# Kernel tuning notes

Measured on AMD Instinct MI355X. Metric: run time of the kernel, lower is better.

## Reference

```python
import jax, jax.numpy as jnp
import numpy as np

B, T, VOCAB, EMBED, HID, TAGS = 64, 512, 30000, 512, 1024, 48
H1, H2 = HID // 2, HID // 4  # per-direction hidden sizes of lstm_1 / lstm_2


def setup_inputs() -> dict:
    key = jax.random.key(0)
    ks = iter(jax.random.split(key, 40))
    def rn(shape, s=0.05):
        return jax.random.normal(next(ks), shape, dtype=jnp.float32) * s
    inp = {
        "sequences": jax.random.randint(next(ks), (B, T), 0, VOCAB),
        "tags": jax.random.randint(next(ks), (B, T), 0, TAGS),
        "mask": jnp.ones((B, T), dtype=bool),
        "h0": rn((2, B, H1), 1.0), "c0": rn((2, B, H1), 1.0),
        "h1": rn((2, B, H2), 1.0), "c1": rn((2, B, H2), 1.0),
        "embed_table": rn((VOCAB, EMBED), 1.0),
        "lin_w": rn((TAGS, 2 * H2)), "lin_b": rn((TAGS,)),
        "transitions": rn((TAGS, TAGS)),
        "start_trans": rn((TAGS,)), "end_trans": rn((TAGS,)),
    }
    for name, (i_dim, h_dim) in {"1f": (EMBED, H1), "1b": (EMBED, H1),
                                 "2f": (2 * H1, H2), "2b": (2 * H1, H2)}.items():
        inp["w_ih" + name] = rn((4 * h_dim, i_dim))
        inp["w_hh" + name] = rn((4 * h_dim, h_dim))
        inp["b_ih" + name] = rn((4 * h_dim,))
        inp["b_hh" + name] = rn((4 * h_dim,))
    return inp


def _lstm_scan(x, h0, c0, w_ih, w_hh, b):
    # x: [T,B,I] time-major; PyTorch gate order i,f,g,o
    def step(carry, x_t):
        h, c = carry
        g = x_t @ w_ih.T + h @ w_hh.T + b  # [B,4H]
        i, f, gg, o = jnp.split(g, 4, axis=-1)
        c = jax.nn.sigmoid(f) * c + jax.nn.sigmoid(i) * jnp.tanh(gg)
        h = jax.nn.sigmoid(o) * jnp.tanh(c)
        return (h, c), h
    _, hs = jax.lax.scan(step, (h0, c0), x)
    return hs  # [T,B,H]


def _bilstm(x, h0, c0, pf, pb):
    hf = _lstm_scan(x, h0[0], c0[0], *pf)
    hb = _lstm_scan(x[::-1], h0[1], c0[1], *pb)[::-1]
    return jnp.concatenate([hf, hb], axis=-1)


def _crf_partition(logits, mask, trans, start, end):
    # logits: [T,B,K], mask: [T,B] bool -> log Z per example [B]
    alpha0 = start[None, :] + logits[0]
    def step(alpha, inp):
        emit, m = inp
        inner = alpha[:, :, None] + trans[None, :, :] + emit[:, None, :]
        new = jax.nn.logsumexp(inner, axis=1)
        return jnp.where(m[:, None], new, alpha), None
    alpha, _ = jax.lax.scan(step, alpha0, (logits[1:], mask[1:]))
    return jax.nn.logsumexp(alpha + end[None, :], axis=-1)


def _crf_joint(logits, tags, mask, trans, start, end):
    # logits: [T,B,K], tags/mask: [T,B] -> gold path score [B]
    mf = mask.astype(logits.dtype)
    bidx = jnp.arange(tags.shape[1])
    emit = jnp.take_along_axis(logits, tags[..., None], axis=-1)[..., 0]  # [T,B]
    score = start[tags[0]]
    score = score + jnp.sum(trans[tags[:-1], tags[1:]] * mf[1:], axis=0)
    score = score + jnp.sum(emit[:-1] * mf[:-1], axis=0)
    last_idx = jnp.sum(mask.astype(jnp.int32), axis=0) - 1
    last_tags = tags[last_idx, bidx]
    score = score + end[last_tags] + logits[-1, bidx, last_tags] * mf[-1]
    return score


def reference(sequences, tags, mask, h0, c0, h1, c1, embed_table, lin_w, lin_b,
              transitions, start_trans, end_trans,
              w_ih1f, w_hh1f, b_ih1f, b_hh1f, w_ih1b, w_hh1b, b_ih1b, b_hh1b,
              w_ih2f, w_hh2f, b_ih2f, b_hh2f, w_ih2b, w_hh2b, b_ih2b, b_hh2b):
    x = embed_table[sequences.T]  # [T,B,E] (time-major, as in get_logits)
    out1 = _bilstm(x, h0, c0,
                   (w_ih1f, w_hh1f, b_ih1f + b_hh1f),
                   (w_ih1b, w_hh1b, b_ih1b + b_hh1b))  # [T,B,HID]
    out2 = _bilstm(out1, h1, c1,
                   (w_ih2f, w_hh2f, b_ih2f + b_hh2f),
                   (w_ih2b, w_hh2b, b_ih2b + b_hh2b))  # [T,B,HID//2]
    logits = out2 @ lin_w.T + lin_b  # [T,B,TAGS]; dropout is identity in eval
    mt, tt = mask.T, tags.T  # [T,B]
    log_z = _crf_partition(logits, mt, transitions, start_trans, end_trans)
    joint = _crf_joint(logits, tt, mt, transitions, start_trans, end_trans)
    return -jnp.sum(joint - log_z)
```

## Files before the change

### kernel.cpp

```cpp
#include <hip/hip_runtime.h>
#include <stdint.h>

#define TT 512
#define BB 64
#define NTAGS 48
#define CH 64

typedef __attribute__((ext_vector_type(8))) short bf16x8;
typedef __attribute__((ext_vector_type(4))) float f32x4;
typedef __attribute__((ext_vector_type(4))) unsigned short u16x4;

__device__ inline unsigned short f2bf(float f) {
  union { float f; unsigned u; } v; v.f = f;
  unsigned r = v.u + 0x7fffu + ((v.u >> 16) & 1u);
  return (unsigned short)(r >> 16);
}
__device__ inline float bf2f(unsigned short u) {
  union { unsigned u; float f; } v; v.u = ((unsigned)u) << 16; return v.f;
}
__device__ inline float sigf(float x) { return 1.0f / (1.0f + __expf(-x)); }
__device__ inline float tanhfast(float x) { return 1.0f - 2.0f / (__expf(2.0f * x) + 1.0f); }

__global__ void k_gather_x(const float* __restrict__ emb, const int* __restrict__ seq,
                           unsigned short* __restrict__ x) {
  size_t i4 = ((size_t)blockIdx.x * 256 + threadIdx.x) * 4;
  int r = (int)(i4 >> 9);
  int k = (int)(i4 & 511);
  int t = r >> 6, b = r & 63;
  int tok = seq[b * TT + t];
  float4 v = *(const float4*)(emb + (size_t)tok * 512 + k);
  unsigned short* dst = x + i4;
  dst[0] = f2bf(v.x); dst[1] = f2bf(v.y); dst[2] = f2bf(v.z); dst[3] = f2bf(v.w);
}

__global__ void k_conv(const float* __restrict__ s, unsigned short* __restrict__ d, int n4) {
  int i = blockIdx.x * 256 + threadIdx.x;
  if (i >= n4) return;
  float4 v = *(const float4*)(s + (size_t)i * 4);
  unsigned short* dst = d + (size_t)i * 4;
  dst[0] = f2bf(v.x); dst[1] = f2bf(v.y); dst[2] = f2bf(v.z); dst[3] = f2bf(v.w);
}

__global__ void k_misc2(const float* __restrict__ h0, const float* __restrict__ h1,
                        const float* __restrict__ c0, const float* __restrict__ c1,
                        const float* __restrict__ bi1f, const float* __restrict__ bh1f,
                        const float* __restrict__ bi1b, const float* __restrict__ bh1b,
                        const float* __restrict__ bi2f, const float* __restrict__ bh2f,
                        const float* __restrict__ bi2b, const float* __restrict__ bh2b,
                        float* __restrict__ bs1, float* __restrict__ bs2,
                        unsigned short* __restrict__ hb1, unsigned short* __restrict__ hb2,
                        float* __restrict__ cb1, float* __restrict__ cb2) {
  int i = blockIdx.x * 256 + threadIdx.x;
  if (i < 4096) { int dd = i >> 11, n = i & 2047; bs1[i] = dd ? (bi1b[n] + bh1b[n]) : (bi1f[n] + bh1f[n]); return; }
  i -= 4096;
  if (i < 2048) { int dd = i >> 10, n = i & 1023; bs2[i] = dd ? (bi2b[n] + bh2b[n]) : (bi2f[n] + bh2f[n]); return; }
  i -= 2048;
  if (i < 65536) { hb1[i] = f2bf(h0[i]); return; }
  i -= 65536;
  if (i < 32768) { hb2[i] = f2bf(h1[i]); return; }
  i -= 32768;
  if (i < 65536) { cb1[i] = c0[i]; return; }
  i -= 65536;
  if (i < 32768) { cb2[i] = c1[i]; return; }
}

template<int KX, int H>
__global__ __launch_bounds__(512) void k_xproj_c(
    const unsigned short* __restrict__ xin,
    const unsigned short* __restrict__ Wih,
    const float* __restrict__ bsum,
    unsigned short* __restrict__ xp, int s0) {
  const int UG = H / 16;
  int wid = blockIdx.x * 8 + (threadIdx.x >> 6);
  const int lane = threadIdx.x & 63;
  const int ug = wid % UG; wid /= UG;
  const int g = wid & 3; wid >>= 2;
  const int dir = wid & 1; wid >>= 1;
  const int sc = wid;
  const int s = s0 + sc;
  const int t = dir ? (TT - 1 - s) : s;
  const int r16 = lane & 15, kg = lane >> 4;
  const int rowg = dir * 4 * H + g * H + ug * 16 + r16;
  const unsigned short* wrow = Wih + (size_t)rowg * KX + kg * 8;
  const float bias = bsum[rowg];
  const unsigned short* xa = xin + (size_t)t * 64 * KX + kg * 8;
  f32x4 A0 = {bias, bias, bias, bias}, A1 = A0, A2 = A0, A3 = A0;
  #pragma unroll
  for (int kc = 0; kc < KX / 128; ++kc) {
    bf16x8 wv_[4], av_[4][4];
    #pragma unroll
    for (int u = 0; u < 4; ++u) {
      const int kk = kc * 4 + u;
      wv_[u] = *(const bf16x8*)(wrow + kk * 32);
      av_[u][0] = *(const bf16x8*)(xa + (size_t)(0 * 16 + r16) * KX + kk * 32);
      av_[u][1] = *(const bf16x8*)(xa + (size_t)(1 * 16 + r16) * KX + kk * 32);
      av_[u][2] = *(const bf16x8*)(xa + (size_t)(2 * 16 + r16) * KX + kk * 32);
      av_[u][3] = *(const bf16x8*)(xa + (size_t)(3 * 16 + r16) * KX + kk * 32);
    }
    #pragma unroll
    for (int u = 0; u < 4; ++u) {
      A0 = __builtin_amdgcn_mfma_f32_16x16x32_bf16(av_[u][0], wv_[u], A0, 0, 0, 0);
      A1 = __builtin_amdgcn_mfma_f32_16x16x32_bf16(av_[u][1], wv_[u], A1, 0, 0, 0);
      A2 = __builtin_amdgcn_mfma_f32_16x16x32_bf16(av_[u][2], wv_[u], A2, 0, 0, 0);
      A3 = __builtin_amdgcn_mfma_f32_16x16x32_bf16(av_[u][3], wv_[u], A3, 0, 0, 0);
    }
  }
  unsigned short* dst = xp + ((((size_t)sc * 2 + dir) * UG + ug) * 4 + g) * 1024 + lane * 4;
  u16x4 s0v = {f2bf(A0[0]), f2bf(A0[1]), f2bf(A0[2]), f2bf(A0[3])};
  u16x4 s1v = {f2bf(A1[0]), f2bf(A1[1]), f2bf(A1[2]), f2bf(A1[3])};
  u16x4 s2v = {f2bf(A2[0]), f2bf(A2[1]), f2bf(A2[2]), f2bf(A2[3])};
  u16x4 s3v = {f2bf(A3[0]), f2bf(A3[1]), f2bf(A3[2]), f2bf(A3[3])};
  *(u16x4*)(dst + 0)   = s0v;
  *(u16x4*)(dst + 256) = s1v;
  *(u16x4*)(dst + 512) = s2v;
  *(u16x4*)(dst + 768) = s3v;
}

template<int H, int NBLKD>
__global__ __launch_bounds__(256, 1) void k_lstm_c(
    const unsigned short* __restrict__ xp,
    const unsigned short* __restrict__ Whh,
    float* __restrict__ cbuf,
    unsigned short* __restrict__ hbuf,
    unsigned short* __restrict__ outp,
    unsigned* __restrict__ arr, int s0) {
  const int UG = H / 16;
  const int dir = blockIdx.x / NBLKD;
  const int ug  = blockIdx.x % NBLKD;
  const int bt = threadIdx.x >> 6, lane = threadIdx.x & 63;
  const int r16 = lane & 15, kg = lane >> 4;

  __shared__ unsigned short Wl[64 * H];
  for (int c = threadIdx.x; c < 64 * (H / 8); c += 256) {
    const int lrow = c / (H / 8), k8 = c % (H / 8);
    bf16x8 v = *(const bf16x8*)(Whh + ((size_t)(dir * 4 * H + (lrow >> 4) * H + ug * 16 + (lrow & 15))) * H + k8 * 8);
    const int addr = ((lrow * H + k8 * 8) * 2) ^ ((lrow & 7) << 4);
    *(bf16x8*)((char*)Wl + addr) = v;
  }

  const int batch0 = bt * 16 + kg * 4;
  float creg[4];
  #pragma unroll
  for (int rr = 0; rr < 4; ++rr)
    creg[rr] = cbuf[((size_t)dir * 64 + batch0 + rr) * H + ug * 16 + r16];

  __syncthreads();

  unsigned* const grp    = arr + (size_t)(dir * 4 + bt) * NBLKD * 4;
  unsigned* const myflag = grp + (size_t)ug * 4;

  auto xpb = [&](int sc) -> const unsigned short* {
    return xp + (((size_t)sc * 2 + dir) * UG + ug) * 4096 + bt * 256 + lane * 4;
  };
  const unsigned short* pb = xpb(0);
  u16x4 px0 = *(const u16x4*)(pb + 0);
  u16x4 px1 = *(const u16x4*)(pb + 1024);
  u16x4 px2 = *(const u16x4*)(pb + 2048);
  u16x4 px3 = *(const u16x4*)(pb + 3072);

  for (int sc = 0; sc < CH; ++sc) {
    const int s = s0 + sc;
    const int p = s & 1;
    f32x4 A0, A1, A2, A3;
    #pragma unroll
    for (int rr = 0; rr < 4; ++rr) {
      A0[rr] = bf2f(px0[rr]);
      A1[rr] = bf2f(px1[rr]);
      A2[rr] = bf2f(px2[rr]);
      A3[rr] = bf2f(px3[rr]);
    }
    if (sc + 1 < CH) {
      pb = xpb(sc + 1);
      px0 = *(const u16x4*)(pb + 0);
      px1 = *(const u16x4*)(pb + 1024);
      px2 = *(const u16x4*)(pb + 2048);
      px3 = *(const u16x4*)(pb + 3072);
    }
    if (s > 0) {
      const unsigned* ap = grp + (size_t)lane * 4;
      const bool act = lane < NBLKD;
      for (;;) {
        unsigned vv = act ? __hip_atomic_load(ap, __ATOMIC_RELAXED, __HIP_MEMORY_SCOPE_AGENT)
                          : 0xffffffffu;
        if (__all(vv >= (unsigned)s)) break;
        __builtin_amdgcn_s_sleep(1);
      }
      asm volatile("" ::: "memory");
    }
    const unsigned short* hrow = hbuf + (((size_t)p * 2 + dir) * 64 + bt * 16 + r16) * H + kg * 8;
    bf16x8 hreg[H / 32];
    #pragma unroll
    for (int kk = 0; kk < H / 32; ++kk) {
      union { bf16x8 v; unsigned long long q[2]; } hu;
      hu.q[0] = __hip_atomic_load((const unsigned long long*)(hrow + kk * 32), __ATOMIC_RELAXED, __HIP_MEMORY_SCOPE_AGENT);
      hu.q[1] = __hip_atomic_load((const unsigned long long*)(hrow + kk * 32 + 4), __ATOMIC_RELAXED, __HIP_MEMORY_SCOPE_AGENT);
      hreg[kk] = hu.v;
    }
    const int sw = (r16 & 7) << 4;
    #pragma unroll
    for (int kk = 0; kk < H / 32; ++kk) {
      bf16x8 w0 = *(const bf16x8*)((const char*)Wl + ((((0 * 16 + r16) * H + kk * 32 + kg * 8) * 2) ^ sw));
      bf16x8 w1 = *(const bf16x8*)((const char*)Wl + ((((1 * 16 + r16) * H + kk * 32 + kg * 8) * 2) ^ sw));
      bf16x8 w2 = *(const bf16x8*)((const char*)Wl + ((((2 * 16 + r16) * H + kk * 32 + kg * 8) * 2) ^ sw));
      bf16x8 w3 = *(const bf16x8*)((const char*)Wl + ((((3 * 16 + r16) * H + kk * 32 + kg * 8) * 2) ^ sw));
      A0 = __builtin_amdgcn_mfma_f32_16x16x32_bf16(hreg[kk], w0, A0, 0, 0, 0);
      A1 = __builtin_amdgcn_mfma_f32_16x16x32_bf16(hreg[kk], w1, A1, 0, 0, 0);
      A2 = __builtin_amdgcn_mfma_f32_16x16x32_bf16(hreg[kk], w2, A2, 0, 0, 0);
      A3 = __builtin_amdgcn_mfma_f32_16x16x32_bf16(hreg[kk], w3, A3, 0, 0, 0);
    }
    const int t = dir ? (TT - 1 - s) : s;
    unsigned short* hw = hbuf + ((size_t)(p ^ 1) * 2 + dir) * 64 * H;
    unsigned short hbv[4];
    #pragma unroll
    for (int rr = 0; rr < 4; ++rr) {
      float cn = sigf(A1[rr]) * creg[rr] + sigf(A0[rr]) * tanhfast(A2[rr]);
      float hn = sigf(A3[rr]) * tanhfast(cn);
      creg[rr] = cn;
      hbv[rr] = f2bf(hn);
      __hip_atomic_store(hw + (size_t)(batch0 + rr) * H + ug * 16 + r16, hbv[rr],
                         __ATOMIC_RELAXED, __HIP_MEMORY_SCOPE_AGENT);
    }
    asm volatile("s_waitcnt vmcnt(0)" ::: "memory");
    if (lane == 0)
      __hip_atomic_store(myflag, (unsigned)(s + 1), __ATOMIC_RELAXED, __HIP_MEMORY_SCOPE_AGENT);
    #pragma unroll
    for (int rr = 0; rr < 4; ++rr)
      outp[((size_t)t * 64 + batch0 + rr) * (2 * H) + dir * H + ug * 16 + r16] = hbv[rr];
  }
  #pragma unroll
  for (int rr = 0; rr < 4; ++rr)
    cbuf[((size_t)dir * 64 + batch0 + rr) * H + ug * 16 + r16] = creg[rr];
}

template<int KX, int H, int NBLKD>
__global__ __launch_bounds__(512, 2) void k_lstm(
    const unsigned short* __restrict__ xin, const unsigned short* __restrict__ Wih,
    const unsigned short* __restrict__ Whh, const float* __restrict__ bsum,
    const float* __restrict__ cinit, unsigned short* __restrict__ hbuf,
    unsigned short* __restrict__ outp, unsigned* __restrict__ arr) {
  const int dir = blockIdx.x / NBLKD;
  const int ug  = blockIdx.x % NBLKD;
  const int wv = threadIdx.x >> 6, lane = threadIdx.x & 63;
  const int r16 = lane & 15, kg = lane >> 4;
  __shared__ unsigned short Wl[64 * H];
  __shared__ float xacc[2][4][4][256];
  __shared__ unsigned done[2];
  __shared__ int ready;
  if (threadIdx.x == 0) { done[0] = 0u; done[1] = 0u; ready = -1; }
  for (int c = threadIdx.x; c < 64 * (H / 8); c += 512) {
    const int lrow = c / (H / 8), k8 = c % (H / 8);
    bf16x8 v = *(const bf16x8*)(Whh + ((size_t)(dir * 4 * H + (lrow >> 4) * H + ug * 16 + (lrow & 15))) * H + k8 * 8);
    const int addr = ((lrow * H + k8 * 8) * 2) ^ ((lrow & 7) << 4);
    *(bf16x8*)((char*)Wl + addr) = v;
  }
  float creg[4];
  auto xgemm = [&](int sn) {
    const int gg = wv - 4;
    const int rowg = dir * 4 * H + gg * H + ug * 16 + r16;
    const unsigned short* wrow = Wih + (size_t)rowg * KX + kg * 8;
    const float bias = bsum[rowg];
    const int t = dir ? (TT - 1 - sn) : sn;
    const unsigned short* xa = xin + (size_t)t * 64 * KX + kg * 8;
    f32x4 A0 = {bias, bias, bias, bias}, A1 = A0, A2 = A0, A3 = A0;
    #pragma unroll
    for (int kc = 0; kc < KX / 128; ++kc) {
      bf16x8 wv_[4], av_[4][4];
      #pragma unroll
      for (int u = 0; u < 4; ++u) {
        const int kk = kc * 4 + u;
        wv_[u] = *(const bf16x8*)(wrow + kk * 32);
        av_[u][0] = *(const bf16x8*)(xa + (size_t)(0 * 16 + r16) * KX + kk * 32);
        av_[u][1] = *(const bf16x8*)(xa + (size_t)(1 * 16 + r16) * KX + kk * 32);
        av_[u][2] = *(const bf16x8*)(xa + (size_t)(2 * 16 + r16) * KX + kk * 32);
        av_[u][3] = *(const bf16x8*)(xa + (size_t)(3 * 16 + r16) * KX + kk * 32);
      }
      #pragma unroll
      for (int u = 0; u < 4; ++u) {
        A0 = __builtin_amdgcn_mfma_f32_16x16x32_bf16(av_[u][0], wv_[u], A0, 0, 0, 0);
        A1 = __builtin_amdgcn_mfma_f32_16x16x32_bf16(av_[u][1], wv_[u], A1, 0, 0, 0);
        A2 = __builtin_amdgcn_mfma_f32_16x16x32_bf16(av_[u][2], wv_[u], A2, 0, 0, 0);
        A3 = __builtin_amdgcn_mfma_f32_16x16x32_bf16(av_[u][3], wv_[u], A3, 0, 0, 0);
      }
    }
    const int p = sn & 1;
    *(f32x4*)&xacc[p][gg][0][lane * 4] = A0;
    *(f32x4*)&xacc[p][gg][1][lane * 4] = A1;
    *(f32x4*)&xacc[p][gg][2][lane * 4] = A2;
    *(f32x4*)&xacc[p][gg][3][lane * 4] = A3;
  };
  if (wv < 4) {
    const int batch0 = wv * 16 + kg * 4;
    #pragma unroll
    for (int rr = 0; rr < 4; ++rr)
      creg[rr] = cinit[((size_t)dir * 64 + batch0 + rr) * H + ug * 16 + r16];
  } else {
    xgemm(0);
  }
  for (int s = 0; s < TT; ++s) {
    __syncthreads();
    if (wv >= 4) {
      if (s + 1 < TT) xgemm(s + 1);
    } else {
      const int p = s & 1;
      const int bt = wv;
      f32x4 A0 = *(const f32x4*)&xacc[p][0][bt][lane * 4];
      f32x4 A1 = *(const f32x4*)&xacc[p][1][bt][lane * 4];
      f32x4 A2 = *(const f32x4*)&xacc[p][2][bt][lane * 4];
      f32x4 A3 = *(const f32x4*)&xacc[p][3][bt][lane * 4];
      const unsigned short* hrow = hbuf + (((size_t)p * 2 + dir) * 64 + bt * 16 + r16) * H + kg * 8;
      if (s > 0) {
        if (wv == 0) {
          const unsigned* ap = arr + ((size_t)dir * NBLKD + lane) * 4;
          const bool act = lane < NBLKD;
          for (;;) {
            unsigned vv = act ? __hip_atomic_load(ap, __ATOMIC_RELAXED, __HIP_MEMORY_SCOPE_AGENT)
                              : 0xffffffffu;
            if (__all(vv >= (unsigned)s)) break;
            __builtin_amdgcn_s_sleep(4);
          }
          if (lane == 0) __hip_atomic_store(&ready, s, __ATOMIC_RELAXED, __HIP_MEMORY_SCOPE_WORKGROUP);
        } else {
          while (__hip_atomic_load(&ready, __ATOMIC_RELAXED, __HIP_MEMORY_SCOPE_WORKGROUP) < s)
            __builtin_amdgcn_s_sleep(1);
        }
        asm volatile("" ::: "memory");
      }
      bf16x8 hreg[H / 32];
      #pragma unroll
      for (int kk = 0; kk < H / 32; ++kk) {
        union { bf16x8 v; unsigned long long q[2]; } hu;
        hu.q[0] = __hip_atomic_load((const unsigned long long*)(hrow + kk * 32), __ATOMIC_RELAXED, __HIP_MEMORY_SCOPE_AGENT);
        hu.q[1] = __hip_atomic_load((const unsigned long long*)(hrow + kk * 32 + 4), __ATOMIC_RELAXED, __HIP_MEMORY_SCOPE_AGENT);
        hreg[kk] = hu.v;
      }
      const int sw = (r16 & 7) << 4;
      #pragma unroll
      for (int kk = 0; kk < H / 32; ++kk) {
        bf16x8 w0 = *(const bf16x8*)((const char*)Wl + ((((0 * 16 + r16) * H + kk * 32 + kg * 8) * 2) ^ sw));
        bf16x8 w1 = *(const bf16x8*)((const char*)Wl + ((((1 * 16 + r16) * H + kk * 32 + kg * 8) * 2) ^ sw));
        bf16x8 w2 = *(const bf16x8*)((const char*)Wl + ((((2 * 16 + r16) * H + kk * 32 + kg * 8) * 2) ^ sw));
        bf16x8 w3 = *(const bf16x8*)((const char*)Wl + ((((3 * 16 + r16) * H + kk * 32 + kg * 8) * 2) ^ sw));
        A0 = __builtin_amdgcn_mfma_f32_16x16x32_bf16(hreg[kk], w0, A0, 0, 0, 0);
        A1 = __builtin_amdgcn_mfma_f32_16x16x32_bf16(hreg[kk], w1, A1, 0, 0, 0);
        A2 = __builtin_amdgcn_mfma_f32_16x16x32_bf16(hreg[kk], w2, A2, 0, 0, 0);
        A3 = __builtin_amdgcn_mfma_f32_16x16x32_bf16(hreg[kk], w3, A3, 0, 0, 0);
      }
      const int t = dir ? (TT - 1 - s) : s;
      const int batch0 = bt * 16 + kg * 4;
      unsigned short* hw = hbuf + ((size_t)(p ^ 1) * 2 + dir) * 64 * H;
      unsigned short hbv[4];
      #pragma unroll
      for (int rr = 0; rr < 4; ++rr) {
        float cn = sigf(A1[rr]) * creg[rr] + sigf(A0[rr]) * tanhfast(A2[rr]);
        float hn = sigf(A3[rr]) * tanhfast(cn);
        creg[rr] = cn;
        hbv[rr] = f2bf(hn);
        __hip_atomic_store(hw + (size_t)(batch0 + rr) * H + ug * 16 + r16, hbv[rr],
                           __ATOMIC_RELAXED, __HIP_MEMORY_SCOPE_AGENT);
      }
      asm volatile("s_waitcnt vmcnt(0)" ::: "memory");
      if (lane == 0) {
        unsigned old = __hip_atomic_fetch_add(&done[p], 1u, __ATOMIC_ACQ_REL, __HIP_MEMORY_SCOPE_WORKGROUP);
        if (old == 3u) {
          done[p] = 0u;
          __hip_atomic_store(arr + ((size_t)dir * NBLKD + ug) * 4, (unsigned)(s + 1),
                             __ATOMIC_RELAXED, __HIP_MEMORY_SCOPE_AGENT);
        }
      }
      #pragma unroll
      for (int rr = 0; rr < 4; ++rr)
        outp[((size_t)t * 64 + batch0 + rr) * (2 * H) + dir * H + ug * 16 + r16] = hbv[rr];
    }
  }
}

__global__ __launch_bounds__(256) void k_linear(const unsigned short* __restrict__ out2,
                                                const unsigned short* __restrict__ wl,
                                                const float* __restrict__ lb,
                                                float* __restrict__ logits) {
  const int wid = blockIdx.x * 4 + (threadIdx.x >> 6);
  const int lane = threadIdx.x & 63;
  const int mt = wid / 3, nt = wid % 3;
  const int r16 = lane & 15, kg = lane >> 4;
  const unsigned short* ar = out2 + ((size_t)mt * 16 + r16) * 512 + kg * 8;
  const unsigned short* br = wl + ((size_t)(nt * 16 + r16)) * 512 + kg * 8;
  f32x4 acc = {0.f, 0.f, 0.f, 0.f};
  #pragma unroll
  for (int kk = 0; kk < 16; ++kk) {
    bf16x8 av = *(const bf16x8*)(ar + kk * 32);
    bf16x8 bv = *(const bf16x8*)(br + kk * 32);
    acc = __builtin_amdgcn_mfma_f32_16x16x32_bf16(av, bv, acc, 0, 0, 0);
  }
  const int col = nt * 16 + r16;
  const float bias = lb[col];
  #pragma unroll
  for (int rr = 0; rr < 4; ++rr) {
    const int m = mt * 16 + kg * 4 + rr;
    logits[(size_t)m * 48 + col] = acc[rr] + bias;
  }
}

__global__ void k_crf_part(const float* __restrict__ logits, const float* __restrict__ trans,
                           const float* __restrict__ start, const float* __restrict__ endt,
                           float* __restrict__ logz) {
  const int b = blockIdx.x;
  const int j = threadIdx.x;
  __shared__ __align__(16) float alpha[2][NTAGS];
  float trj[NTAGS];
  if (j < NTAGS) {
    #pragma unroll
    for (int i = 0; i < NTAGS; ++i) trj[i] = trans[i * NTAGS + j];
    alpha[0][j] = start[j] + logits[(size_t)b * NTAGS + j];
  }
  float cur = (j < NTAGS) ? logits[((size_t)1 * BB + b) * NTAGS + j] : 0.f;
  __syncthreads();
  for (int t = 1; t < TT; ++t) {
    float nxt = (j < NTAGS && t + 1 < TT) ? logits[((size_t)(t + 1) * BB + b) * NTAGS + j] : 0.f;
    const int p = (t - 1) & 1;
    float newv = 0.f;
    if (j < NTAGS) {
      float v[NTAGS];
      const float4* ap = (const float4*)&alpha[p][0];
      #pragma unroll
      for (int q = 0; q < NTAGS / 4; ++q) {
        float4 v4 = ap[q];
        v[4 * q + 0] = v4.x + trj[4 * q + 0];
        v[4 * q + 1] = v4.y + trj[4 * q + 1];
        v[4 * q + 2] = v4.z + trj[4 * q + 2];
        v[4 * q + 3] = v4.w + trj[4 * q + 3];
      }
      float m0[24], m1[12], m2[6], m3[3];
      #pragma unroll
      for (int i = 0; i < 24; ++i) m0[i] = fmaxf(v[2 * i], v[2 * i + 1]);
      #pragma unroll
      for (int i = 0; i < 12; ++i) m1[i] = fmaxf(m0[2 * i], m0[2 * i + 1]);
      #pragma unroll
      for (int i = 0; i < 6; ++i) m2[i] = fmaxf(m1[2 * i], m1[2 * i + 1]);
      #pragma unroll
      for (int i = 0; i < 3; ++i) m3[i] = fmaxf(m2[2 * i], m2[2 * i + 1]);
      const float m = fmaxf(fmaxf(m3[0], m3[1]), m3[2]);
      float e[NTAGS];
      #pragma unroll
      for (int i = 0; i < NTAGS; ++i) e[i] = __expf(v[i] - m);
      float s0[24], s1[12], s2[6], s3[3];
      #pragma unroll
      for (int i = 0; i < 24; ++i) s0[i] = e[2 * i] + e[2 * i + 1];
      #pragma unroll
      for (int i = 0; i < 12; ++i) s1[i] = s0[2 * i] + s0[2 * i + 1];
      #pragma unroll
      for (int i = 0; i < 6; ++i) s2[i] = s1[2 * i] + s1[2 * i + 1];
      #pragma unroll
      for (int i = 0; i < 3; ++i) s3[i] = s2[2 * i] + s2[2 * i + 1];
      const float ssum = s3[0] + s3[1] + s3[2];
      newv = m + __logf(ssum) + cur;
    }
    if (j < NTAGS) alpha[p ^ 1][j] = newv;
    __syncthreads();
    cur = nxt;
  }
  float vfin = (j < NTAGS) ? alpha[(TT - 1) & 1][j] + endt[j] : -1e30f;
  float m = vfin;
  for (int o = 32; o; o >>= 1) m = fmaxf(m, __shfl_xor(m, o));
  float e = (j < NTAGS) ? __expf(vfin - m) : 0.f;
  for (int o = 32; o; o >>= 1) e += __shfl_xor(e, o);
  if (j == 0) logz[b] = m + __logf(e);
}

__global__ void k_crf_joint(const float* __restrict__ logits, const int* __restrict__ tags,
                            const float* __restrict__ trans, const float* __restrict__ start,
                            const float* __restrict__ endt, float* __restrict__ joint) {
  const int b = blockIdx.x;
  const int tid = threadIdx.x;
  float p = 0.f;
  for (int t = tid; t < TT - 1; t += 64) {
    const int tt = tags[b * TT + t], tn = tags[b * TT + t + 1];
    p += trans[tt * NTAGS + tn] + logits[((size_t)t * BB + b) * 48 + tt];
  }
  for (int o = 32; o; o >>= 1) p += __shfl_xor(p, o);
  if (tid == 0) {
    const int t0 = tags[b * TT];
    const int tl = tags[b * TT + TT - 1];
    p += start[t0] + endt[tl] + logits[((size_t)(TT - 1) * BB + b) * 48 + tl];
    joint[b] = p;
  }
}

__global__ void k_final(const float* __restrict__ joint, const float* __restrict__ logz,
                        float* __restrict__ out) {
  const int tid = threadIdx.x;
  float v = joint[tid] - logz[tid];
  for (int o = 32; o; o >>= 1) v += __shfl_xor(v, o);
  if (tid == 0) out[0] = -v;
}

#define X_OFF    ((size_t)0)
#define WIH1_OFF ((size_t)33554432)
#define WHH1_OFF ((size_t)37748736)
#define WIH2_OFF ((size_t)41943040)
#define WHH2_OFF ((size_t)46137344)
#define WL_OFF   ((size_t)47185920)
#define BS1_OFF  ((size_t)47235072)
#define BS2_OFF  ((size_t)47251456)
#define OUT1_OFF ((size_t)47259648)
#define OUT2_OFF ((size_t)114368512)
#define LG_OFF   ((size_t)147922944)
#define HB1_OFF  ((size_t)154214400)
#define HB2_OFF  ((size_t)154476544)
#define LZ_OFF   ((size_t)154607616)
#define JT_OFF   ((size_t)154607872)
#define BAR_OFF  ((size_t)154608128)
#define WS_NEED  ((size_t)154624512)
#define CB1_OFF  ((size_t)154624512)
#define CB2_OFF  ((size_t)154886656)
#define XP_OFF   ((size_t)155017728)
#define WS_XP    ((size_t)171794944)

extern "C" void kernel_launch(void* const* d_in, const int* in_sizes, int n_in,
                              void* d_out, int out_size, void* d_ws, size_t ws_size,
                              hipStream_t stream) {
  if (ws_size < WS_NEED) return;
  const int*   seq    = (const int*)d_in[0];
  const int*   tags   = (const int*)d_in[1];
  const float* h0     = (const float*)d_in[3];
  const float* c0     = (const float*)d_in[4];
  const float* h1     = (const float*)d_in[5];
  const float* c1     = (const float*)d_in[6];
  const float* emb    = (const float*)d_in[7];
  const float* lin_w  = (const float*)d_in[8];
  const float* lin_b  = (const float*)d_in[9];
  const float* trans  = (const float*)d_in[10];
  const float* start_t= (const float*)d_in[11];
  const float* end_t  = (const float*)d_in[12];
  const float* wih1f  = (const float*)d_in[13];
  const float* whh1f  = (const float*)d_in[14];
  const float* bih1f  = (const float*)d_in[15];
  const float* bhh1f  = (const float*)d_in[16];
  const float* wih1b  = (const float*)d_in[17];
  const float* whh1b  = (const float*)d_in[18];
  const float* bih1b  = (const float*)d_in[19];
  const float* bhh1b  = (const float*)d_in[20];
  const float* wih2f  = (const float*)d_in[21];
  const float* whh2f  = (const float*)d_in[22];
  const float* bih2f  = (const float*)d_in[23];
  const float* bhh2f  = (const float*)d_in[24];
  const float* wih2b  = (const float*)d_in[25];
  const float* whh2b  = (const float*)d_in[26];
  const float* bih2b  = (const float*)d_in[27];
  const float* bhh2b  = (const float*)d_in[28];

  char* ws = (char*)d_ws;
  unsigned short* x    = (unsigned short*)(ws + X_OFF);
  unsigned short* Wih1 = (unsigned short*)(ws + WIH1_OFF);
  unsigned short* Whh1 = (unsigned short*)(ws + WHH1_OFF);
  unsigned short* Wih2 = (unsigned short*)(ws + WIH2_OFF);
  unsigned short* Whh2 = (unsigned short*)(ws + WHH2_OFF);
  unsigned short* WL   = (unsigned short*)(ws + WL_OFF);
  float*          bs1  = (float*)(ws + BS1_OFF);
  float*          bs2  = (float*)(ws + BS2_OFF);
  unsigned short* out1 = (unsigned short*)(ws + OUT1_OFF);
  unsigned short* out2 = (unsigned short*)(ws + OUT2_OFF);
  float*          lg   = (float*)(ws + LG_OFF);
  unsigned short* hb1  = (unsigned short*)(ws + HB1_OFF);
  unsigned short* hb2  = (unsigned short*)(ws + HB2_OFF);
  float*          lz   = (float*)(ws + LZ_OFF);
  float*          jt   = (float*)(ws + JT_OFF);
  unsigned*       bars = (unsigned*)(ws + BAR_OFF);
  const bool big = ws_size >= WS_XP;
  float*          cb1  = big ? (float*)(ws + CB1_OFF) : nullptr;
  float*          cb2  = big ? (float*)(ws + CB2_OFF) : nullptr;
  unsigned short* xp   = big ? (unsigned short*)(ws + XP_OFF) : nullptr;

  hipMemsetAsync(bars, 0, 16384, stream);

  k_gather_x<<<16384, 256, 0, stream>>>(emb, seq, x);
  k_conv<<<1024, 256, 0, stream>>>(wih1f, Wih1,                 262144);
  k_conv<<<1024, 256, 0, stream>>>(wih1b, Wih1 + 2048 * 512,    262144);
  k_conv<<<1024, 256, 0, stream>>>(whh1f, Whh1,                 262144);
  k_conv<<<1024, 256, 0, stream>>>(whh1b, Whh1 + 2048 * 512,    262144);
  k_conv<<<1024, 256, 0, stream>>>(wih2f, Wih2,                 262144);
  k_conv<<<1024, 256, 0, stream>>>(wih2b, Wih2 + 1024 * 1024,   262144);
  k_conv<<<256, 256, 0, stream>>>(whh2f, Whh2,                  65536);
  k_conv<<<256, 256, 0, stream>>>(whh2b, Whh2 + 1024 * 256,     65536);
  k_conv<<<24, 256, 0, stream>>>(lin_w, WL,                     6144);

  if (big) {
    k_misc2<<<792, 256, 0, stream>>>(h0, h1, c0, c1, bih1f, bhh1f, bih1b, bhh1b,
                                     bih2f, bhh2f, bih2b, bhh2b, bs1, bs2, hb1, hb2, cb1, cb2);
    for (int c = 0; c < TT / CH; ++c) {
      k_xproj_c<512, 512><<<2048, 512, 0, stream>>>(x, Wih1, bs1, xp, c * CH);
      k_lstm_c<512, 32><<<64, 256, 0, stream>>>(xp, Whh1, cb1, hb1, out1, bars, c * CH);
    }
    for (int c = 0; c < TT / CH; ++c) {
      k_xproj_c<1024, 256><<<1024, 512, 0, stream>>>(out1, Wih2, bs2, xp, c * CH);
      k_lstm_c<256, 16><<<32, 256, 0, stream>>>(xp, Whh2, cb2, hb2, out2, bars + 2048, c * CH);
    }
  } else {
    k_misc2<<<792, 256, 0, stream>>>(h0, h1, c0, c1, bih1f, bhh1f, bih1b, bhh1b,
                                     bih2f, bhh2f, bih2b, bhh2b, bs1, bs2, hb1, hb2,
                                     (float*)(ws + LG_OFF), (float*)(ws + LG_OFF + 262144));
    k_lstm<512, 512, 32><<<64, 512, 0, stream>>>(x, Wih1, Whh1, bs1, c0, hb1, out1, bars);
    k_lstm<1024, 256, 16><<<32, 512, 0, stream>>>(out1, Wih2, Whh2, bs2, c1, hb2, out2, bars + 1024);
  }

  k_linear<<<1536, 256, 0, stream>>>(out2, WL, lin_b, lg);
  k_crf_part<<<64, 64, 0, stream>>>(lg, trans, start_t, end_t, lz);
  k_crf_joint<<<64, 64, 0, stream>>>(lg, tags, trans, start_t, end_t, jt);
  k_final<<<1, 64, 0, stream>>>(jt, lz, (float*)d_out);
}
```

Measured before the change: 7.704 ms.

## Fuse next-chunk input projection into LSTM recurrence kernel and tag hidden state with step

The recurrence kernel and the input projection for the next time chunk now share one launch. Extra blocks beyond the recurrent ones compute the next chunk's projections into a double-buffered area while the persistent blocks run the sequential steps at raised priority. The per-block flag barrier is replaced by hidden-state words that carry the step index in their upper 16 bits, so consumers spin directly on the data. This removes the separate flag store, the waitcnt and the flag polling, at the cost of doubling hidden-state storage and needing more workspace. The projection blocks also compete with the latency-critical recurrent blocks for memory bandwidth.

```diff
diff --git a/kernel.cpp b/kernel.cpp
--- a/kernel.cpp
+++ b/kernel.cpp
@@ -49,7 +49,8 @@
                         const float* __restrict__ bi2b, const float* __restrict__ bh2b,
                         float* __restrict__ bs1, float* __restrict__ bs2,
                         unsigned short* __restrict__ hb1, unsigned short* __restrict__ hb2,
-                        float* __restrict__ cb1, float* __restrict__ cb2) {
+                        float* __restrict__ cb1, float* __restrict__ cb2,
+                        unsigned* __restrict__ hb1u, unsigned* __restrict__ hb2u) {
   int i = blockIdx.x * 256 + threadIdx.x;
   if (i < 4096) { int dd = i >> 11, n = i & 2047; bs1[i] = dd ? (bi1b[n] + bh1b[n]) : (bi1f[n] + bh1f[n]); return; }
   i -= 4096;
@@ -62,14 +63,16 @@
   if (i < 65536) { cb1[i] = c0[i]; return; }
   i -= 65536;
   if (i < 32768) { cb2[i] = c1[i]; return; }
+  i -= 32768;
+  if (i < 65536) { if (hb1u) hb1u[i] = (unsigned)f2bf(h0[i]); return; }
+  i -= 65536;
+  if (i < 32768) { if (hb2u) hb2u[i] = (unsigned)f2bf(h1[i]); return; }
 }
 
 template<int KX, int H>
 __global__ __launch_bounds__(512) void k_xproj_c(
-    const unsigned short* __restrict__ xin,
-    const unsigned short* __restrict__ Wih,
-    const float* __restrict__ bsum,
-    unsigned short* __restrict__ xp, int s0) {
+    const unsigned short* __restrict__ xin, const unsigned short* __restrict__ Wih,
+    const float* __restrict__ bsum, unsigned short* __restrict__ xp, int s0) {
   const int UG = H / 16;
   int wid = blockIdx.x * 8 + (threadIdx.x >> 6);
   const int lane = threadIdx.x & 63;
@@ -116,15 +119,70 @@
   *(u16x4*)(dst + 768) = s3v;
 }
 
-template<int H, int NBLKD>
-__global__ __launch_bounds__(256, 1) void k_lstm_c(
-    const unsigned short* __restrict__ xp,
+template<int KX, int H, int NBLKD>
+__global__ __launch_bounds__(256, 1) void k_fused(
+    const unsigned short* __restrict__ xin,
+    const unsigned short* __restrict__ Wih,
+    const float* __restrict__ bsum,
+    unsigned short* __restrict__ xpw,
+    const unsigned short* __restrict__ xpr,
     const unsigned short* __restrict__ Whh,
     float* __restrict__ cbuf,
-    unsigned short* __restrict__ hbuf,
+    unsigned* __restrict__ hbu,
     unsigned short* __restrict__ outp,
-    unsigned* __restrict__ arr, int s0) {
+    int s0, int xs0) {
   const int UG = H / 16;
+  const int NL = 2 * NBLKD;
+
+  if ((int)blockIdx.x >= NL) {
+    if (!xpw) return;
+    const int wv = threadIdx.x >> 6, lane = threadIdx.x & 63;
+    int wid = ((int)blockIdx.x - NL) * 4 + wv;
+    const int ug = wid % UG; wid /= UG;
+    const int g = wid & 3; wid >>= 2;
+    const int dir = wid & 1; wid >>= 1;
+    const int sc = wid;
+    const int s = xs0 + sc;
+    const int t = dir ? (TT - 1 - s) : s;
+    const int r16 = lane & 15, kg = lane >> 4;
+    const int rowg = dir * 4 * H + g * H + ug * 16 + r16;
+    const unsigned short* wrow = Wih + (size_t)rowg * KX + kg * 8;
+    const float bias = bsum[rowg];
+    const unsigned short* xa = xin + (size_t)t * 64 * KX + kg * 8;
+    f32x4 A0 = {bias, bias, bias, bias}, A1 = A0, A2 = A0, A3 = A0;
+    #pragma unroll
+    for (int kc = 0; kc < KX / 128; ++kc) {
+      bf16x8 wv_[4], av_[4][4];
+      #pragma unroll
+      for (int u = 0; u < 4; ++u) {
+        const int kk = kc * 4 + u;
+        wv_[u] = *(const bf16x8*)(wrow + kk * 32);
+        av_[u][0] = *(const bf16x8*)(xa + (size_t)(0 * 16 + r16) * KX + kk * 32);
+        av_[u][1] = *(const bf16x8*)(xa + (size_t)(1 * 16 + r16) * KX + kk * 32);
+        av_[u][2] = *(const bf16x8*)(xa + (size_t)(2 * 16 + r16) * KX + kk * 32);
+        av_[u][3] = *(const bf16x8*)(xa + (size_t)(3 * 16 + r16) * KX + kk * 32);
+      }
+      #pragma unroll
+      for (int u = 0; u < 4; ++u) {
+        A0 = __builtin_amdgcn_mfma_f32_16x16x32_bf16(av_[u][0], wv_[u], A0, 0, 0, 0);
+        A1 = __builtin_amdgcn_mfma_f32_16x16x32_bf16(av_[u][1], wv_[u], A1, 0, 0, 0);
+        A2 = __builtin_amdgcn_mfma_f32_16x16x32_bf16(av_[u][2], wv_[u], A2, 0, 0, 0);
+        A3 = __builtin_amdgcn_mfma_f32_16x16x32_bf16(av_[u][3], wv_[u], A3, 0, 0, 0);
+      }
+    }
+    unsigned short* dst = xpw + ((((size_t)sc * 2 + dir) * UG + ug) * 4 + g) * 1024 + lane * 4;
+    u16x4 s0v = {f2bf(A0[0]), f2bf(A0[1]), f2bf(A0[2]), f2bf(A0[3])};
+    u16x4 s1v = {f2bf(A1[0]), f2bf(A1[1]), f2bf(A1[2]), f2bf(A1[3])};
+    u16x4 s2v = {f2bf(A2[0]), f2bf(A2[1]), f2bf(A2[2]), f2bf(A2[3])};
+    u16x4 s3v = {f2bf(A3[0]), f2bf(A3[1]), f2bf(A3[2]), f2bf(A3[3])};
+    *(u16x4*)(dst + 0)   = s0v;
+    *(u16x4*)(dst + 256) = s1v;
+    *(u16x4*)(dst + 512) = s2v;
+    *(u16x4*)(dst + 768) = s3v;
+    return;
+  }
+
+  __builtin_amdgcn_s_setprio(1);
   const int dir = blockIdx.x / NBLKD;
   const int ug  = blockIdx.x % NBLKD;
   const int bt = threadIdx.x >> 6, lane = threadIdx.x & 63;
@@ -146,11 +204,8 @@
 
   __syncthreads();
 
-  unsigned* const grp    = arr + (size_t)(dir * 4 + bt) * NBLKD * 4;
-  unsigned* const myflag = grp + (size_t)ug * 4;
-
   auto xpb = [&](int sc) -> const unsigned short* {
-    return xp + (((size_t)sc * 2 + dir) * UG + ug) * 4096 + bt * 256 + lane * 4;
+    return xpr + (((size_t)sc * 2 + dir) * UG + ug) * 4096 + bt * 256 + lane * 4;
   };
   const unsigned short* pb = xpb(0);
   u16x4 px0 = *(const u16x4*)(pb + 0);
@@ -176,40 +231,49 @@
       px2 = *(const u16x4*)(pb + 2048);
       px3 = *(const u16x4*)(pb + 3072);
     }
-    if (s > 0) {
-      const unsigned* ap = grp + (size_t)lane * 4;
-      const bool act = lane < NBLKD;
-      for (;;) {
-        unsigned vv = act ? __hip_atomic_load(ap, __ATOMIC_RELAXED, __HIP_MEMORY_SCOPE_AGENT)
-                          : 0xffffffffu;
-        if (__all(vv >= (unsigned)s)) break;
-        __builtin_amdgcn_s_sleep(1);
-      }
-      asm volatile("" ::: "memory");
-    }
-    const unsigned short* hrow = hbuf + (((size_t)p * 2 + dir) * 64 + bt * 16 + r16) * H + kg * 8;
-    bf16x8 hreg[H / 32];
+    const unsigned* hrowu = hbu + (((size_t)p * 2 + dir) * 64 + bt * 16 + r16) * H + kg * 8;
+    unsigned hr[H / 32][4];
+    const unsigned exp_hi = (unsigned)s << 16;
+    for (;;) {
+      unsigned bad = 0u;
+      #pragma unroll
+      for (int kk = 0; kk < H / 32; ++kk) {
+        unsigned long long q0 = __hip_atomic_load((const unsigned long long*)(hrowu + kk * 32 + 0), __ATOMIC_RELAXED, __HIP_MEMORY_SCOPE_AGENT);
+        unsigned long long q1 = __hip_atomic_load((const unsigned long long*)(hrowu + kk * 32 + 2), __ATOMIC_RELAXED, __HIP_MEMORY_SCOPE_AGENT);
+        unsigned long long q2 = __hip_atomic_load((const unsigned long long*)(hrowu + kk * 32 + 4), __ATOMIC_RELAXED, __HIP_MEMORY_SCOPE_AGENT);
+        unsigned long long q3 = __hip_atomic_load((const unsigned long long*)(hrowu + kk * 32 + 6), __ATOMIC_RELAXED, __HIP_MEMORY_SCOPE_AGENT);
+        unsigned w0 = (unsigned)q0, w1 = (unsigned)(q0 >> 32);
+        unsigned w2 = (unsigned)q1, w3 = (unsigned)(q1 >> 32);
+        unsigned w4 = (unsigned)q2, w5 = (unsigned)(q2 >> 32);
+        unsigned w6 = (unsigned)q3, w7 = (unsigned)(q3 >> 32);
+        bad |= (w0 ^ exp_hi) | (w1 ^ exp_hi) | (w2 ^ exp_hi) | (w3 ^ exp_hi)
+             | (w4 ^ exp_hi) | (w5 ^ exp_hi) | (w6 ^ exp_hi) | (w7 ^ exp_hi);
+        hr[kk][0] = (w0 & 0xFFFFu) | (w1 << 16);
+        hr[kk][1] = (w2 & 0xFFFFu) | (w3 << 16);
+        hr[kk][2] = (w4 & 0xFFFFu) | (w5 << 16);
+        hr[kk][3] = (w6 & 0xFFFFu) | (w7 << 16);
+      }
+      if (__all((bad & 0xFFFF0000u) == 0u)) break;
+      __builtin_amdgcn_s_sleep(1);
+    }
+    const int sw = (r16 & 7) << 4;
     #pragma unroll
     for (int kk = 0; kk < H / 32; ++kk) {
-      union { bf16x8 v; unsigned long long q[2]; } hu;
-      hu.q[0] = __hip_atomic_load((const unsigned long long*)(hrow + kk * 32), __ATOMIC_RELAXED, __HIP_MEMORY_SCOPE_AGENT);
-      hu.q[1] = __hip_atomic_load((const unsigned long long*)(hrow + kk * 32 + 4), __ATOMIC_RELAXED, __HIP_MEMORY_SCOPE_AGENT);
-      hreg[kk] = hu.v;
-    }
-    const int sw = (r16 & 7) << 4;
-    #pragma unroll
-    for (int kk = 0; kk < H / 32; ++kk) {
+      union { unsigned u[4]; bf16x8 v; } hu;
+      hu.u[0] = hr[kk][0]; hu.u[1] = hr[kk][1]; hu.u[2] = hr[kk][2]; hu.u[3] = hr[kk][3];
+      bf16x8 av = hu.v;
       bf16x8 w0 = *(const bf16x8*)((const char*)Wl + ((((0 * 16 + r16) * H + kk * 32 + kg * 8) * 2) ^ sw));
       bf16x8 w1 = *(const bf16x8*)((const char*)Wl + ((((1 * 16 + r16) * H + kk * 32 + kg * 8) * 2) ^ sw));
       bf16x8 w2 = *(const bf16x8*)((const char*)Wl + ((((2 * 16 + r16) * H + kk * 32 + kg * 8) * 2) ^ sw));
       bf16x8 w3 = *(const bf16x8*)((const char*)Wl + ((((3 * 16 + r16) * H + kk * 32 + kg * 8) * 2) ^ sw));
-      A0 = __builtin_amdgcn_mfma_f32_16x16x32_bf16(hreg[kk], w0, A0, 0, 0, 0);
-      A1 = __builtin_amdgcn_mfma_f32_16x16x32_bf16(hreg[kk], w1, A1, 0, 0, 0);
-      A2 = __builtin_amdgcn_mfma_f32_16x16x32_bf16(hreg[kk], w2, A2, 0, 0, 0);
-      A3 = __builtin_amdgcn_mfma_f32_16x16x32_bf16(hreg[kk], w3, A3, 0, 0, 0);
+      A0 = __builtin_amdgcn_mfma_f32_16x16x32_bf16(av, w0, A0, 0, 0, 0);
+      A1 = __builtin_amdgcn_mfma_f32_16x16x32_bf16(av, w1, A1, 0, 0, 0);
+      A2 = __builtin_amdgcn_mfma_f32_16x16x32_bf16(av, w2, A2, 0, 0, 0);
+      A3 = __builtin_amdgcn_mfma_f32_16x16x32_bf16(av, w3, A3, 0, 0, 0);
     }
     const int t = dir ? (TT - 1 - s) : s;
-    unsigned short* hw = hbuf + ((size_t)(p ^ 1) * 2 + dir) * 64 * H;
+    unsigned* hwu = hbu + ((size_t)(p ^ 1) * 2 + dir) * 64 * H;
+    const unsigned st = ((unsigned)(s + 1)) << 16;
     unsigned short hbv[4];
     #pragma unroll
     for (int rr = 0; rr < 4; ++rr) {
@@ -217,12 +281,9 @@
       float hn = sigf(A3[rr]) * tanhfast(cn);
       creg[rr] = cn;
       hbv[rr] = f2bf(hn);
-      __hip_atomic_store(hw + (size_t)(batch0 + rr) * H + ug * 16 + r16, hbv[rr],
-                         __ATOMIC_RELAXED, __HIP_MEMORY_SCOPE_AGENT);
-    }
-    asm volatile("s_waitcnt vmcnt(0)" ::: "memory");
-    if (lane == 0)
-      __hip_atomic_store(myflag, (unsigned)(s + 1), __ATOMIC_RELAXED, __HIP_MEMORY_SCOPE_AGENT);
+      __hip_atomic_store(hwu + (size_t)(batch0 + rr) * H + ug * 16 + r16,
+                         st | (unsigned)hbv[rr], __ATOMIC_RELAXED, __HIP_MEMORY_SCOPE_AGENT);
+    }
     #pragma unroll
     for (int rr = 0; rr < 4; ++rr)
       outp[((size_t)t * 64 + batch0 + rr) * (2 * H) + dir * H + ug * 16 + r16] = hbv[rr];
@@ -512,8 +573,12 @@
 #define WS_NEED  ((size_t)154624512)
 #define CB1_OFF  ((size_t)154624512)
 #define CB2_OFF  ((size_t)154886656)
-#define XP_OFF   ((size_t)155017728)
-#define WS_XP    ((size_t)171794944)
+#define HB1U_OFF ((size_t)155017728)
+#define HB2U_OFF ((size_t)155542016)
+#define XP_OFF   ((size_t)155804160)
+#define XPSZ     ((size_t)16777216)
+#define WS_C     ((size_t)(XP_OFF + XPSZ))
+#define WS_F     ((size_t)(XP_OFF + 2 * XPSZ))
 
 extern "C" void kernel_launch(void* const* d_in, const int* in_sizes, int n_in,
                               void* d_out, int out_size, void* d_ws, size_t ws_size,
@@ -565,12 +630,20 @@
   float*          lz   = (float*)(ws + LZ_OFF);
   float*          jt   = (float*)(ws + JT_OFF);
   unsigned*       bars = (unsigned*)(ws + BAR_OFF);
-  const bool big = ws_size >= WS_XP;
-  float*          cb1  = big ? (float*)(ws + CB1_OFF) : nullptr;
-  float*          cb2  = big ? (float*)(ws + CB2_OFF) : nullptr;
-  unsigned short* xp   = big ? (unsigned short*)(ws + XP_OFF) : nullptr;
+  const bool chunked = ws_size >= WS_C;
+  const bool fused   = ws_size >= WS_F;
+  float*          cb1  = chunked ? (float*)(ws + CB1_OFF) : (float*)(ws + LG_OFF);
+  float*          cb2  = chunked ? (float*)(ws + CB2_OFF) : (float*)(ws + LG_OFF + 262144);
+  unsigned*       hb1u = chunked ? (unsigned*)(ws + HB1U_OFF) : nullptr;
+  unsigned*       hb2u = chunked ? (unsigned*)(ws + HB2U_OFF) : nullptr;
+  unsigned short* xpA  = chunked ? (unsigned short*)(ws + XP_OFF) : nullptr;
+  unsigned short* xpB  = fused   ? (unsigned short*)(ws + XP_OFF + XPSZ) : xpA;
 
   hipMemsetAsync(bars, 0, 16384, stream);
+  if (chunked) {
+    hipMemsetAsync(hb1u, 0, 524288, stream);
+    hipMemsetAsync(hb2u, 0, 262144, stream);
+  }
 
   k_gather_x<<<16384, 256, 0, stream>>>(emb, seq, x);
   k_conv<<<1024, 256, 0, stream>>>(wih1f, Wih1,                 262144);
@@ -582,22 +655,40 @@
   k_conv<<<256, 256, 0, stream>>>(whh2f, Whh2,                  65536);
   k_conv<<<256, 256, 0, stream>>>(whh2b, Whh2 + 1024 * 256,     65536);
   k_conv<<<24, 256, 0, stream>>>(lin_w, WL,                     6144);
-
-  if (big) {
-    k_misc2<<<792, 256, 0, stream>>>(h0, h1, c0, c1, bih1f, bhh1f, bih1b, bhh1b,
-                                     bih2f, bhh2f, bih2b, bhh2b, bs1, bs2, hb1, hb2, cb1, cb2);
+  k_misc2<<<1176, 256, 0, stream>>>(h0, h1, c0, c1, bih1f, bhh1f, bih1b, bhh1b,
+                                    bih2f, bhh2f, bih2b, bhh2b, bs1, bs2, hb1, hb2,
+                                    cb1, cb2, hb1u, hb2u);
+
+  if (chunked) {
+    k_xproj_c<512, 512><<<2048, 512, 0, stream>>>(x, Wih1, bs1, xpA, 0);
     for (int c = 0; c < TT / CH; ++c) {
-      k_xproj_c<512, 512><<<2048, 512, 0, stream>>>(x, Wih1, bs1, xp, c * CH);
-      k_lstm_c<512, 32><<<64, 256, 0, stream>>>(xp, Whh1, cb1, hb1, out1, bars, c * CH);
-    }
+      unsigned short* cur = (c & 1) ? xpB : xpA;
+      unsigned short* nxt = (c & 1) ? xpA : xpB;
+      if (fused && c + 1 < TT / CH) {
+        k_fused<512, 512, 32><<<64 + 4096, 256, 0, stream>>>(
+            x, Wih1, bs1, nxt, cur, Whh1, cb1, hb1u, out1, c * CH, (c + 1) * CH);
+      } else {
+        if (!fused && c + 1 < TT / CH)
+          k_xproj_c<512, 512><<<2048, 512, 0, stream>>>(x, Wih1, bs1, nxt, (c + 1) * CH);
+        k_fused<512, 512, 32><<<64, 256, 0, stream>>>(
+            x, Wih1, bs1, nullptr, cur, Whh1, cb1, hb1u, out1, c * CH, 0);
+      }
+    }
+    k_xproj_c<1024, 256><<<1024, 512, 0, stream>>>(out1, Wih2, bs2, xpA, 0);
     for (int c = 0; c < TT / CH; ++c) {
-      k_xproj_c<1024, 256><<<1024, 512, 0, stream>>>(out1, Wih2, bs2, xp, c * CH);
-      k_lstm_c<256, 16><<<32, 256, 0, stream>>>(xp, Whh2, cb2, hb2, out2, bars + 2048, c * CH);
+      unsigned short* cur = (c & 1) ? xpB : xpA;
+      unsigned short* nxt = (c & 1) ? xpA : xpB;
+      if (fused && c + 1 < TT / CH) {
+        k_fused<1024, 256, 16><<<32 + 2048, 256, 0, stream>>>(
+            out1, Wih2, bs2, nxt, cur, Whh2, cb2, hb2u, out2, c * CH, (c + 1) * CH);
+      } else {
+        if (!fused && c + 1 < TT / CH)
+          k_xproj_c<1024, 256><<<1024, 512, 0, stream>>>(out1, Wih2, bs2, nxt, (c + 1) * CH);
+        k_fused<1024, 256, 16><<<32, 256, 0, stream>>>(
+            out1, Wih2, bs2, nullptr, cur, Whh2, cb2, hb2u, out2, c * CH, 0);
+      }
     }
   } else {
-    k_misc2<<<792, 256, 0, stream>>>(h0, h1, c0, c1, bih1f, bhh1f, bih1b, bhh1b,
-                                     bih2f, bhh2f, bih2b, bhh2b, bs1, bs2, hb1, hb2,
-                                     (float*)(ws + LG_OFF), (float*)(ws + LG_OFF + 262144));
     k_lstm<512, 512, 32><<<64, 512, 0, stream>>>(x, Wih1, Whh1, bs1, c0, hb1, out1, bars);
     k_lstm<1024, 256, 16><<<32, 512, 0, stream>>>(out1, Wih2, Whh2, bs2, c1, hb2, out2, bars + 1024);
   }
```

Result: slower. 13.27 ms (+72.2%).
